# Performance work log

Measured on AMD Instinct MI355X. Metric: run time of the kernel, lower is better.

The kernel has to match this reference:

```python
import jax, jax.numpy as jnp
import numpy as np

WINDOW = 60
DEPTH = 3
HIDDEN = 256
LN_EPS = 1e-5


def _lyndon_indices(d):
    # Lyndon words over alphabet {0..d-1}, lengths 2 and 3, lexicographic order
    # (signatory mode='words' extracts expanded-logsig coefficients at Lyndon words).
    i2 = np.array([(i, j) for i in range(d) for j in range(d) if (i, j) < (j, i)], dtype=np.int32)
    i3 = np.array([(i, j, k) for i in range(d) for j in range(d) for k in range(d)
                   if (i, j, k) < (j, k, i) and (i, j, k) < (k, i, j)], dtype=np.int32)
    return i2, i3


def _logsig_features(x):
    # x: [b, s, c] -> logsignature of time-augmented sliding windows: [b*s, sig_channels]
    b, s, c = x.shape
    d = c + 1
    # replicate-padded sliding windows via clipped gather (matches F.pad replicate + unfold)
    pos = jnp.clip(jnp.arange(s)[:, None] + jnp.arange(WINDOW)[None, :] - (WINDOW - 1), 0, s - 1)
    windows = x[:, pos, :]                                   # [b, s, W, c]
    t = jnp.linspace(0.0, 1.0, WINDOW, dtype=x.dtype)        # time augmentation channel
    t_b = jnp.broadcast_to(t[None, None, :, None], (b, s, WINDOW, 1))
    aug = jnp.concatenate([t_b, windows], axis=-1).reshape(b * s, WINDOW, d)
    N = b * s
    # basepoint=True: prepend zero point -> increments include the first point itself
    inc = jnp.diff(aug, axis=1, prepend=jnp.zeros((N, 1, d), aug.dtype))  # [N, W, d]
    inc_t = jnp.transpose(inc, (1, 0, 2))                    # [W, N, d]

    def chen_step(carry, v):
        S1, S2, S3 = carry
        vv = jnp.einsum('ni,nj->nij', v, v)
        vvv = jnp.einsum('nij,nk->nijk', vv, v)
        nS3 = S3 + jnp.einsum('nij,nk->nijk', S2, v) \
                 + 0.5 * jnp.einsum('ni,njk->nijk', S1, vv) + vvv / 6.0
        nS2 = S2 + jnp.einsum('ni,nj->nij', S1, v) + 0.5 * vv
        nS1 = S1 + v
        return (nS1, nS2, nS3), None

    init = (jnp.zeros((N, d), x.dtype), jnp.zeros((N, d, d), x.dtype), jnp.zeros((N, d, d, d), x.dtype))
    (S1, S2, S3), _ = jax.lax.scan(chen_step, init, inc_t)
    # log in truncated tensor algebra: log(1+x) = x - x^2/2 + x^3/3
    L1 = S1
    L2 = S2 - 0.5 * jnp.einsum('ni,nj->nij', S1, S1)
    L3 = (S3 - 0.5 * (jnp.einsum('ni,njk->nijk', S1, S2) + jnp.einsum('nij,nk->nijk', S2, S1))
          + jnp.einsum('ni,nj,nk->nijk', S1, S1, S1) / 3.0)
    i2, i3 = _lyndon_indices(d)
    f2 = L2[:, i2[:, 0], i2[:, 1]]
    f3 = L3[:, i3[:, 0], i3[:, 1], i3[:, 2]]
    return jnp.concatenate([L1, f2, f3], axis=-1)            # [N, sig_channels]


def setup_inputs() -> dict:
    key = jax.random.key(0)
    ks = jax.random.split(key, 5)
    b, s, c = 8, 2048, 8
    d = c + 1
    sig_channels = d + (d * d - d) // 2 + (d ** 3 - d) // 3  # 285 for d=9
    h2 = 2 * HIDDEN
    x = jax.random.normal(ks[0], (b, s, c), dtype=jnp.float32)
    w1 = jax.random.normal(ks[1], (sig_channels, h2), dtype=jnp.float32) / np.sqrt(sig_channels)
    b1 = jnp.zeros((h2,), jnp.float32)
    ln_g = jnp.ones((h2,), jnp.float32)
    ln_b = jnp.zeros((h2,), jnp.float32)
    w2 = jax.random.normal(ks[2], (h2, HIDDEN), dtype=jnp.float32) / np.sqrt(h2)
    b2 = jnp.zeros((HIDDEN,), jnp.float32)
    return {"x": x, "w1": w1, "b1": b1, "ln_g": ln_g, "ln_b": ln_b, "w2": w2, "b2": b2}


def reference(x, w1, b1, ln_g, ln_b, w2, b2):
    b, s, _ = x.shape
    feats = _logsig_features(x)                              # [b*s, sig_channels]
    h = jax.nn.gelu(feats @ w1 + b1, approximate=False)      # torch default GELU (erf)
    mu = jnp.mean(h, axis=-1, keepdims=True)
    var = jnp.var(h, axis=-1, keepdims=True)
    h = (h - mu) / jnp.sqrt(var + LN_EPS) * ln_g + ln_b      # LayerNorm; Dropout is eval no-op
    out = h @ w2 + b2
    return out.reshape(b, s, -1)
```

## Files before the change

### kernel.cpp

```cpp
#include <hip/hip_runtime.h>
#include <hip/hip_bf16.h>
#include <cstdint>
#include <cstddef>

typedef short short8 __attribute__((ext_vector_type(8)));
typedef float f32x4 __attribute__((ext_vector_type(4)));
typedef float f32x2 __attribute__((ext_vector_type(2)));

#define NS    2048
#define KPAD  288
#define H2    512
#define HID   256
#define WPB   7
#define SBLK  293
#define KLDS1 296
#define KLDS2 520

#define MFMA(a,b,c) __builtin_amdgcn_mfma_f32_16x16x32_bf16((a),(b),(c),0,0,0)

__device__ __forceinline__ float geluf(float x) {
    return 0.5f * x * (1.0f + erff(x * 0.70710678118654752f));
}
__device__ __forceinline__ f32x4 shfl4(f32x4 v, int d) {
    f32x4 r;
    r[0] = __shfl_xor(v[0], d); r[1] = __shfl_xor(v[1], d);
    r[2] = __shfl_xor(v[2], d); r[3] = __shfl_xor(v[3], d);
    return r;
}

struct Tbl3 { short col[729]; };
static constexpr Tbl3 make_tbl3() {
    Tbl3 t{};
    for (int x = 0; x < 729; ++x) t.col[x] = -1;
    int r = 0;
    for (int i = 0; i < 9; ++i)
        for (int j = 0; j < 9; ++j)
            for (int k = 0; k < 9; ++k) {
                bool lt1 = (i < j) || (i == j && (j < k || (j == k && k < i)));
                bool lt2 = (i < k) || (i == k && (j < i || (j == i && k < j)));
                if (lt1 && lt2) { t.col[(i*9+j)*9+k] = (short)(45 + r); ++r; }
            }
    return t;
}
static constexpr Tbl3 TBL3 = make_tbl3();

#define SIG_STEP(VA_,VB_,VC_) { \
    const float hh = 0.5f * S1i + vi * (1.0f/6.0f); \
    const float ra = S2ra + hh * (VA_); \
    const float rb = S2rb + hh * (VB_); \
    const float rc = S2rc + hh * (VC_); \
    const f32x2 ra2 = {ra, ra}, rb2 = {rb, rb}, rc2 = {rc, rc}; \
    S3sa += ra * v0; S3pa0 += ra2*vp0; S3pa1 += ra2*vp1; S3pa2 += ra2*vp2; S3pa3 += ra2*vp3; \
    S3sb += rb * v0; S3pb0 += rb2*vp0; S3pb1 += rb2*vp1; S3pb2 += rb2*vp2; S3pb3 += rb2*vp3; \
    S3sc += rc * v0; S3pc0 += rc2*vp0; S3pc1 += rc2*vp1; S3pc2 += rc2*vp2; S3pc3 += rc2*vp3; \
    const float aa = S1i + 0.5f * vi; \
    S2ra += aa * (VA_); S2rb += aa * (VB_); S2rc += aa * (VC_); \
    S1i += vi; }

#define SIG_MAIN(VA_,VB_,VC_) { \
    { const float* xr = &X[(g0 - lo) * 8]; \
      const float4 e0 = *(const float4*)xr; \
      const float4 e1 = *(const float4*)(xr + 4); \
      const float rs = xr[ioff]; \
      const float v0 = 0.0f; \
      const f32x2 vp0 = {e0.x, e0.y}, vp1 = {e0.z, e0.w}, vp2 = {e1.x, e1.y}, vp3 = {e1.z, e1.w}; \
      const float vi = (ci == 0) ? 0.0f : rs; \
      SIG_STEP(VA_,VB_,VC_) } \
    const float* pd = &PD[(sm59 + 1 - lo + 59) * 8]; \
    float4 d0 = *(const float4*)pd; \
    float4 d1 = *(const float4*)(pd + 4); \
    float rn = pd[ioff]; \
    _Pragma("unroll 2") \
    for (int j = 1; j < 60; ++j) { \
      const float4 e0 = d0; const float4 e1 = d1; const float rs = rn; \
      pd += 8; \
      d0 = *(const float4*)pd; d1 = *(const float4*)(pd + 4); rn = pd[ioff]; \
      const float v0 = DT; \
      const f32x2 vp0 = {e0.x, e0.y}, vp1 = {e0.z, e0.w}, vp2 = {e1.x, e1.y}, vp3 = {e1.z, e1.w}; \
      const float vi = (ci == 0) ? DT : rs; \
      SIG_STEP(VA_,VB_,VC_) \
    } }

#define SIG_ST(RA,RB,RC) \
    if (act) { \
        if ((RA) == 0) S1buf[widx * 9 + ci] = S1i; \
        float* sb = &S2buf[widx * 81 + ci * 9]; \
        sb[RA] = S2ra; sb[RB] = S2rb; sb[RC] = S2rc; \
    }

#define S3EL0(SL) S3s##SL
#define S3EL1(SL) S3p##SL##0[0]
#define S3EL2(SL) S3p##SL##0[1]
#define S3EL3(SL) S3p##SL##1[0]
#define S3EL4(SL) S3p##SL##1[1]
#define S3EL5(SL) S3p##SL##2[0]
#define S3EL6(SL) S3p##SL##2[1]
#define S3EL7(SL) S3p##SL##3[0]
#define S3EL8(SL) S3p##SL##3[1]

#define SIG_E2(SL,J2) if (ci < (J2)) { \
    const float val2 = S2r##SL - 0.5f * S1i * s1v##J2; \
    const int col2 = 9 + ci*8 - (ci*(ci-1))/2 + ((J2) - ci - 1); \
    frow[col2] = __float2bfloat16(val2); }

#define SIG_E3(SL,R,K) { const int col3 = TBL3.col[tb + (R)*9 + (K)]; \
    if (col3 >= 0) { \
        const float val3 = S3EL##K(SL) \
            - 0.5f * (S1i * S2w[(R)*9+(K)] + S2r##SL * s1v##K) \
            + S1i * s1v##R * s1v##K * (1.0f/3.0f); \
        frow[col3] = __float2bfloat16(val3); } }

#define SIG_E3R(SL,R) SIG_E3(SL,R,0) SIG_E3(SL,R,1) SIG_E3(SL,R,2) SIG_E3(SL,R,3) \
    SIG_E3(SL,R,4) SIG_E3(SL,R,5) SIG_E3(SL,R,6) SIG_E3(SL,R,7) SIG_E3(SL,R,8)

#define SIG_EMIT(RA,RB,RC) \
    if (act) { \
        if ((RA) == 0) { \
            frow[ci] = __float2bfloat16(S1i); \
            if (ci == 0) { \
                const __hip_bfloat16 z16 = __float2bfloat16(0.0f); \
                frow[285] = z16; frow[286] = z16; frow[287] = z16; \
            } \
        } \
        SIG_E2(a,RA) SIG_E2(b,RB) SIG_E2(c,RC) \
        SIG_E3R(a,RA) SIG_E3R(b,RB) SIG_E3R(c,RC) \
    }

__global__ __launch_bounds__(192) __attribute__((amdgpu_waves_per_eu(1, 6)))
void sig_kernel(const float* __restrict__ x, __hip_bfloat16* __restrict__ feats) {
    __shared__ __align__(16) float X[66 * 8];
    __shared__ __align__(16) float PD[126 * 8];
    __shared__ float S2buf[WPB * 81];
    __shared__ float S1buf[WPB * 9];

    const int blk = blockIdx.x;
    const int b   = blk / SBLK;
    const int s0  = (blk % SBLK) * WPB;
    const int lo  = (s0 - 59 > 0) ? (s0 - 59) : 0;
    const int hi  = (s0 + WPB - 1 < NS - 1) ? (s0 + WPB - 1) : (NS - 1);
    const int nrow = hi - lo + 1;
    const int tid = threadIdx.x;

    {
        const float4* src = (const float4*)(x + ((size_t)b * NS + lo) * 8);
        float4* X4 = (float4*)X;
        const int n4 = nrow * 2;
        for (int t = tid; t < n4; t += 192) X4[t] = src[t];
    }
    __syncthreads();
    {
        const float4* X4 = (const float4*)X;
        float4* PD4 = (float4*)PD;
        for (int t = tid; t < 252; t += 192) {
            const int p = t >> 1;
            const int r = p - 59;
            float4 dv = {0.f, 0.f, 0.f, 0.f};
            if (r > 0 && r < nrow) {
                const float4 a = X4[t - 118], bb = X4[t - 120];
                dv.x = a.x - bb.x; dv.y = a.y - bb.y; dv.z = a.z - bb.z; dv.w = a.w - bb.w;
            }
            PD4[t] = dv;
        }
    }
    __syncthreads();

    const int t3    = tid >> 6;
    const int lt    = tid & 63;
    const int widx0 = lt / 9;
    const int ci    = lt - widx0 * 9;
    const bool act  = (lt < 63) && (s0 + widx0 < NS);
    const int widx  = (widx0 < WPB - 1) ? widx0 : WPB - 1;
    int s = s0 + widx; if (s > NS - 1) s = NS - 1;

    float S3sa=0.f, S3sb=0.f, S3sc=0.f;
    f32x2 S3pa0={0.f,0.f},S3pa1={0.f,0.f},S3pa2={0.f,0.f},S3pa3={0.f,0.f};
    f32x2 S3pb0={0.f,0.f},S3pb1={0.f,0.f},S3pb2={0.f,0.f},S3pb3={0.f,0.f};
    f32x2 S3pc0={0.f,0.f},S3pc1={0.f,0.f},S3pc2={0.f,0.f},S3pc3={0.f,0.f};
    float S2ra=0.f, S2rb=0.f, S2rc=0.f;
    float S1i = 0.f;
    const int ioff = (ci > 0) ? (ci - 1) : 0;
    const int sm59 = s - 59;
    const int g0   = (sm59 > 0) ? sm59 : 0;
    const float DT = 1.0f / 59.0f;

    if (t3 == 0)      { SIG_MAIN(v0,   e0.x, e0.y) }
    else if (t3 == 1) { SIG_MAIN(e0.z, e0.w, e1.x) }
    else              { SIG_MAIN(e1.y, e1.z, e1.w) }

    if (t3 == 0)      { SIG_ST(0,1,2) }
    else if (t3 == 1) { SIG_ST(3,4,5) }
    else              { SIG_ST(6,7,8) }
    __syncthreads();

    const float* s1p = &S1buf[widx * 9];
    const float s1v0=s1p[0], s1v1=s1p[1], s1v2=s1p[2], s1v3=s1p[3], s1v4=s1p[4];
    const float s1v5=s1p[5], s1v6=s1p[6], s1v7=s1p[7], s1v8=s1p[8];
    const float* S2w = &S2buf[widx * 81];
    const int tb = ci * 81;
    __hip_bfloat16* frow = feats + (size_t)(b * NS + s) * KPAD;

    if (t3 == 0)      { SIG_EMIT(0,1,2) }
    else if (t3 == 1) { SIG_EMIT(3,4,5) }
    else              { SIG_EMIT(6,7,8) }
}

__global__ void convert_w1(const float* __restrict__ w1, __hip_bfloat16* __restrict__ w1T) {
    const int n = blockIdx.x;
    const int k = threadIdx.x;
    const float v = (k < 285) ? w1[(size_t)k * H2 + n] : 0.0f;
    w1T[(size_t)n * KPAD + k] = __float2bfloat16(v);
}
__global__ void convert_w2g(const float* __restrict__ w2, const float* __restrict__ lng,
                            const float* __restrict__ lnb, const float* __restrict__ b2,
                            __hip_bfloat16* __restrict__ w2g, float* __restrict__ gw,
                            float* __restrict__ cvec) {
    const int n = blockIdx.x, k = threadIdx.x;
    const float wv = w2[(size_t)k * HID + n];
    const float a = lng[k] * wv;
    const float c = lnb[k] * wv;
    w2g[(size_t)n * H2 + k] = __float2bfloat16(a);
    float ra = a, rc = c;
#pragma unroll
    for (int d = 1; d < 64; d <<= 1) { ra += __shfl_xor(ra, d); rc += __shfl_xor(rc, d); }
    __shared__ float r1[8], r2[8];
    const int wv_ = k >> 6, ln = k & 63;
    if (ln == 0) { r1[wv_] = ra; r2[wv_] = rc; }
    __syncthreads();
    if (k == 0) {
        float sa = 0.f, sc = 0.f;
#pragma unroll
        for (int i = 0; i < 8; ++i) { sa += r1[i]; sc += r2[i]; }
        gw[n] = sa; cvec[n] = sc + b2[n];
    }
}

__global__ __launch_bounds__(256) __attribute__((amdgpu_waves_per_eu(1, 4)))
void gemm1_kernel(const __hip_bfloat16* __restrict__ feats,
                  const __hip_bfloat16* __restrict__ w1T,
                  const float* __restrict__ b1,
                  __hip_bfloat16* __restrict__ h1,
                  float* __restrict__ stats) {
    __shared__ __align__(16) __hip_bfloat16 ldsB[64 * KLDS1];
    const int tid  = threadIdx.x;
    const int wave = tid >> 6;
    const int lane = tid & 63;
    const int quad = lane >> 4;
    const int l16  = lane & 15;
    const int m0   = blockIdx.x * 128 + wave * 32;
    const int n0   = blockIdx.y * 64;
    const int nb   = blockIdx.y;

    for (int c = tid; c < 64 * 36; c += 256) {
        const int n = c / 36, k8 = c - n * 36;
        *(short8*)(ldsB + n * KLDS1 + k8 * 8) =
            *(const short8*)(w1T + (size_t)(n0 + n) * KPAD + k8 * 8);
    }
    __syncthreads();

    const __hip_bfloat16* a0 = feats + (size_t)(m0 + l16) * KPAD + quad * 8;
    const __hip_bfloat16* a1 = feats + (size_t)(m0 + 16 + l16) * KPAD + quad * 8;
    const __hip_bfloat16* bb = ldsB + l16 * KLDS1 + quad * 8;

    f32x4 acc00={0,0,0,0},acc01={0,0,0,0},acc02={0,0,0,0},acc03={0,0,0,0};
    f32x4 acc10={0,0,0,0},acc11={0,0,0,0},acc12={0,0,0,0},acc13={0,0,0,0};
#pragma unroll 1
    for (int kt = 0; kt < 9; ++kt) {
        const int ko = kt * 32;
        const short8 av0 = *(const short8*)(a0 + ko);
        const short8 av1 = *(const short8*)(a1 + ko);
        const short8 bv0 = *(const short8*)(bb + ko);
        const short8 bv1 = *(const short8*)(bb + 16 * KLDS1 + ko);
        const short8 bv2 = *(const short8*)(bb + 32 * KLDS1 + ko);
        const short8 bv3 = *(const short8*)(bb + 48 * KLDS1 + ko);
        acc00 = MFMA(av0, bv0, acc00); acc01 = MFMA(av0, bv1, acc01);
        acc02 = MFMA(av0, bv2, acc02); acc03 = MFMA(av0, bv3, acc03);
        acc10 = MFMA(av1, bv0, acc10); acc11 = MFMA(av1, bv1, acc11);
        acc12 = MFMA(av1, bv2, acc12); acc13 = MFMA(av1, bv3, acc13);
    }

    const float bias0 = b1[n0 +  0 + l16];
    const float bias1 = b1[n0 + 16 + l16];
    const float bias2 = b1[n0 + 32 + l16];
    const float bias3 = b1[n0 + 48 + l16];
#define G1G(A,B) { A[0]=geluf(A[0]+B); A[1]=geluf(A[1]+B); A[2]=geluf(A[2]+B); A[3]=geluf(A[3]+B); }
    G1G(acc00,bias0) G1G(acc01,bias1) G1G(acc02,bias2) G1G(acc03,bias3)
    G1G(acc10,bias0) G1G(acc11,bias1) G1G(acc12,bias2) G1G(acc13,bias3)
#undef G1G

    f32x4 s0 = acc00 + acc01 + acc02 + acc03;
    f32x4 q0 = acc00*acc00 + acc01*acc01 + acc02*acc02 + acc03*acc03;
    f32x4 s1 = acc10 + acc11 + acc12 + acc13;
    f32x4 q1 = acc10*acc10 + acc11*acc11 + acc12*acc12 + acc13*acc13;
    s0 += shfl4(s0,1); q0 += shfl4(q0,1); s1 += shfl4(s1,1); q1 += shfl4(q1,1);
    s0 += shfl4(s0,2); q0 += shfl4(q0,2); s1 += shfl4(s1,2); q1 += shfl4(q1,2);
    s0 += shfl4(s0,4); q0 += shfl4(q0,4); s1 += shfl4(s1,4); q1 += shfl4(q1,4);
    s0 += shfl4(s0,8); q0 += shfl4(q0,8); s1 += shfl4(s1,8); q1 += shfl4(q1,8);
    if (l16 == 0) {
#pragma unroll
        for (int r = 0; r < 4; ++r) {
            const int r0 = m0 + quad * 4 + r;
            stats[r0 * 16 + nb] = s0[r]; stats[r0 * 16 + 8 + nb] = q0[r];
            const int r1 = r0 + 16;
            stats[r1 * 16 + nb] = s1[r]; stats[r1 * 16 + 8 + nb] = q1[r];
        }
    }

    {
        __hip_bfloat16* hp = h1 + (size_t)(m0 + quad * 4) * H2;
        const int c0 = n0 + l16;
#pragma unroll
        for (int r = 0; r < 4; ++r) {
            hp[(size_t)r * H2 + c0     ] = __float2bfloat16(acc00[r]);
            hp[(size_t)r * H2 + c0 + 16] = __float2bfloat16(acc01[r]);
            hp[(size_t)r * H2 + c0 + 32] = __float2bfloat16(acc02[r]);
            hp[(size_t)r * H2 + c0 + 48] = __float2bfloat16(acc03[r]);
        }
        __hip_bfloat16* hp2 = hp + (size_t)16 * H2;
#pragma unroll
        for (int r = 0; r < 4; ++r) {
            hp2[(size_t)r * H2 + c0     ] = __float2bfloat16(acc10[r]);
            hp2[(size_t)r * H2 + c0 + 16] = __float2bfloat16(acc11[r]);
            hp2[(size_t)r * H2 + c0 + 32] = __float2bfloat16(acc12[r]);
            hp2[(size_t)r * H2 + c0 + 48] = __float2bfloat16(acc13[r]);
        }
    }
}

__global__ __launch_bounds__(256) __attribute__((amdgpu_waves_per_eu(1, 4)))
void gemm2_kernel(const __hip_bfloat16* __restrict__ h1,
                  const __hip_bfloat16* __restrict__ w2g,
                  const float* __restrict__ stats,
                  const float* __restrict__ gw,
                  const float* __restrict__ cvec,
                  float* __restrict__ out) {
    __shared__ __align__(16) __hip_bfloat16 ldsB[32 * KLDS2];
    const int tid  = threadIdx.x;
    const int wave = tid >> 6;
    const int lane = tid & 63;
    const int quad = lane >> 4;
    const int l16  = lane & 15;
    const int m0   = blockIdx.x * 128 + wave * 32;
    const int n0   = blockIdx.y * 32;

    for (int c = tid; c < 32 * 64; c += 256) {
        const int n = c >> 6, k8 = c & 63;
        *(short8*)(ldsB + n * KLDS2 + k8 * 8) =
            *(const short8*)(w2g + (size_t)(n0 + n) * H2 + k8 * 8);
    }
    __syncthreads();

    const __hip_bfloat16* a0 = h1 + (size_t)(m0 + l16) * H2 + quad * 8;
    const __hip_bfloat16* a1 = h1 + (size_t)(m0 + 16 + l16) * H2 + quad * 8;
    const __hip_bfloat16* bb = ldsB + l16 * KLDS2 + quad * 8;

    f32x4 acc00={0,0,0,0},acc01={0,0,0,0},acc10={0,0,0,0},acc11={0,0,0,0};
#pragma unroll 1
    for (int kt = 0; kt < 16; ++kt) {
        const int ko = kt * 32;
        const short8 av0 = *(const short8*)(a0 + ko);
        const short8 av1 = *(const short8*)(a1 + ko);
        const short8 bv0 = *(const short8*)(bb + ko);
        const short8 bv1 = *(const short8*)(bb + 16 * KLDS2 + ko);
        acc00 = MFMA(av0, bv0, acc00); acc01 = MFMA(av0, bv1, acc01);
        acc10 = MFMA(av1, bv0, acc10); acc11 = MFMA(av1, bv1, acc11);
    }

    const int c0 = n0 + l16, c1 = c0 + 16;
    const float gw0 = gw[c0], gw1 = gw[c1];
    const float cv0 = cvec[c0], cv1 = cvec[c1];
#define G2EP(mf) { \
    const int rbase = m0 + (mf)*16 + quad*4; \
    _Pragma("unroll") \
    for (int r = 0; r < 4; ++r) { \
        const int row = rbase + r; \
        const float4 sA = *(const float4*)&stats[row*16]; \
        const float4 sB = *(const float4*)&stats[row*16+4]; \
        const float4 qA = *(const float4*)&stats[row*16+8]; \
        const float4 qB = *(const float4*)&stats[row*16+12]; \
        const float su = sA.x+sA.y+sA.z+sA.w + sB.x+sB.y+sB.z+sB.w; \
        const float qu = qA.x+qA.y+qA.z+qA.w + qB.x+qB.y+qB.z+qB.w; \
        const float mu = su * (1.0f/512.0f); \
        const float rsv = rsqrtf(qu*(1.0f/512.0f) - mu*mu + 1e-5f); \
        out[(size_t)row*HID + c0] = rsv*(acc##mf##0[r] - mu*gw0) + cv0; \
        out[(size_t)row*HID + c1] = rsv*(acc##mf##1[r] - mu*gw1) + cv1; \
    } }
    G2EP(0) G2EP(1)
#undef G2EP
}

extern "C" void kernel_launch(void* const* d_in, const int* in_sizes, int n_in,
                              void* d_out, int out_size, void* d_ws, size_t ws_size,
                              hipStream_t stream) {
    const float* x   = (const float*)d_in[0];
    const float* w1  = (const float*)d_in[1];
    const float* b1  = (const float*)d_in[2];
    const float* lng = (const float*)d_in[3];
    const float* lnb = (const float*)d_in[4];
    const float* w2  = (const float*)d_in[5];
    const float* b2  = (const float*)d_in[6];
    float* out = (float*)d_out;

    char* ws = (char*)d_ws;
    __hip_bfloat16* feats = (__hip_bfloat16*)(ws);
    __hip_bfloat16* h1    = (__hip_bfloat16*)(ws + 9437184);
    __hip_bfloat16* w1T   = (__hip_bfloat16*)(ws + 26214400);
    __hip_bfloat16* w2g   = (__hip_bfloat16*)(ws + 26509312);
    float*          gw    = (float*)(ws + 26771456);
    float*          cvec  = (float*)(ws + 26775552);
    float*          stats = (float*)(ws + 26779648);

    convert_w1<<<dim3(512), dim3(288), 0, stream>>>(w1, w1T);
    convert_w2g<<<dim3(256), dim3(512), 0, stream>>>(w2, lng, lnb, b2, w2g, gw, cvec);
    sig_kernel<<<dim3(8 * SBLK), dim3(192), 0, stream>>>(x, feats);
    gemm1_kernel<<<dim3(128, 8), dim3(256), 0, stream>>>(feats, w1T, b1, h1, stats);
    gemm2_kernel<<<dim3(128, 8), dim3(256), 0, stream>>>(h1, w2g, stats, gw, cvec, out);
}
```

Before: 167.1 us.

## Merge weight conversion kernels and fully unroll GEMM and signature loops

Combines the two weight-conversion kernels into one launch, with block ranges split between the w1 transpose and the w2 gamma-fold, so one kernel launch goes away. It also fully unrolls the K loops in both GEMM kernels and raises the unroll factor of the signature recurrence loop from 2 to 4. These aim to cut launch overhead and loop overhead and to let the compiler schedule loads ahead of MFMAs. The cost is higher register pressure, which could lower occupancy. The merged kernel also leaves threads idle in the w1 blocks because the block size rises to 512.

```diff
diff --git a/kernel.cpp b/kernel.cpp
--- a/kernel.cpp
+++ b/kernel.cpp
@@ -70,7 +70,7 @@
     float4 d0 = *(const float4*)pd; \
     float4 d1 = *(const float4*)(pd + 4); \
     float rn = pd[ioff]; \
-    _Pragma("unroll 2") \
+    _Pragma("unroll 4") \
     for (int j = 1; j < 60; ++j) { \
       const float4 e0 = d0; const float4 e1 = d1; const float rs = rn; \
       pd += 8; \
@@ -204,17 +204,22 @@
     else              { SIG_EMIT(6,7,8) }
 }
 
-__global__ void convert_w1(const float* __restrict__ w1, __hip_bfloat16* __restrict__ w1T) {
-    const int n = blockIdx.x;
+__global__ __launch_bounds__(512) void convert_weights(
+        const float* __restrict__ w1, const float* __restrict__ w2,
+        const float* __restrict__ lng, const float* __restrict__ lnb,
+        const float* __restrict__ b2,
+        __hip_bfloat16* __restrict__ w1T, __hip_bfloat16* __restrict__ w2g,
+        float* __restrict__ gw, float* __restrict__ cvec) {
+    const int blk = blockIdx.x;
     const int k = threadIdx.x;
-    const float v = (k < 285) ? w1[(size_t)k * H2 + n] : 0.0f;
-    w1T[(size_t)n * KPAD + k] = __float2bfloat16(v);
-}
-__global__ void convert_w2g(const float* __restrict__ w2, const float* __restrict__ lng,
-                            const float* __restrict__ lnb, const float* __restrict__ b2,
-                            __hip_bfloat16* __restrict__ w2g, float* __restrict__ gw,
-                            float* __restrict__ cvec) {
-    const int n = blockIdx.x, k = threadIdx.x;
+    if (blk < 512) {
+        if (k < KPAD) {
+            const float v = (k < 285) ? w1[(size_t)k * H2 + blk] : 0.0f;
+            w1T[(size_t)blk * KPAD + k] = __float2bfloat16(v);
+        }
+        return;
+    }
+    const int n = blk - 512;
     const float wv = w2[(size_t)k * HID + n];
     const float a = lng[k] * wv;
     const float c = lnb[k] * wv;
@@ -263,7 +268,7 @@
 
     f32x4 acc00={0,0,0,0},acc01={0,0,0,0},acc02={0,0,0,0},acc03={0,0,0,0};
     f32x4 acc10={0,0,0,0},acc11={0,0,0,0},acc12={0,0,0,0},acc13={0,0,0,0};
-#pragma unroll 1
+#pragma unroll
     for (int kt = 0; kt < 9; ++kt) {
         const int ko = kt * 32;
         const short8 av0 = *(const short8*)(a0 + ko);
@@ -354,7 +359,7 @@
     const __hip_bfloat16* bb = ldsB + l16 * KLDS2 + quad * 8;
 
     f32x4 acc00={0,0,0,0},acc01={0,0,0,0},acc10={0,0,0,0},acc11={0,0,0,0};
-#pragma unroll 1
+#pragma unroll
     for (int kt = 0; kt < 16; ++kt) {
         const int ko = kt * 32;
         const short8 av0 = *(const short8*)(a0 + ko);
@@ -409,8 +414,8 @@
     float*          cvec  = (float*)(ws + 26775552);
     float*          stats = (float*)(ws + 26779648);
 
-    convert_w1<<<dim3(512), dim3(288), 0, stream>>>(w1, w1T);
-    convert_w2g<<<dim3(256), dim3(512), 0, stream>>>(w2, lng, lnb, b2, w2g, gw, cvec);
+    convert_weights<<<dim3(768), dim3(512), 0, stream>>>(w1, w2, lng, lnb, b2,
+                                                         w1T, w2g, gw, cvec);
     sig_kernel<<<dim3(8 * SBLK), dim3(192), 0, stream>>>(x, feats);
     gemm1_kernel<<<dim3(128, 8), dim3(256), 0, stream>>>(feats, w1T, b1, h1, stats);
     gemm2_kernel<<<dim3(128, 8), dim3(256), 0, stream>>>(h1, w2g, stats, gw, cvec, out);
```

Result: no change. 164.8 us (-1.4%).
